# Performance work log

Hardware: AMD Instinct MI355X
Metric: run time of the kernel (lower is better)

The kernel has to match this reference:

```python
import jax, jax.numpy as jnp
import numpy as np

HEADS = 4
DIM_HEAD = 32
GROUPS = 32  # min(256//4, 32)
EPS = 1e-5


def setup_inputs() -> dict:
    key = jax.random.key(0)
    ks = jax.random.split(key, 5)
    B, C, H, W = 16, 256, 64, 64
    CD, HC, WC = 512, 32, 32
    hid = HEADS * DIM_HEAD  # 128
    return {
        "x": jax.random.normal(ks[0], (B, C, H, W), jnp.float32),
        "cond": jax.random.normal(ks[1], (B, CD, HC, WC), jnp.float32),
        "gn_w": jnp.ones((C,), jnp.float32),
        "gn_b": jnp.zeros((C,), jnp.float32),
        "w_q": jax.random.normal(ks[2], (hid, C), jnp.float32) * 0.05,
        "b_q": jnp.zeros((hid,), jnp.float32),
        "w_kv": jax.random.normal(ks[3], (2 * hid, CD), jnp.float32) * 0.05,
        "b_kv": jnp.zeros((2 * hid,), jnp.float32),
        "w_out": jax.random.normal(ks[4], (C, hid), jnp.float32) * 0.05,
        "b_out": jnp.zeros((C,), jnp.float32),
    }


def _group_norm(x, w, b):
    # x: (B, C, H, W); normalize per group over (channels-in-group, H, W)
    B, C, H, W = x.shape
    xg = x.reshape(B, GROUPS, C // GROUPS, H, W)
    mu = jnp.mean(xg, axis=(2, 3, 4), keepdims=True)
    var = jnp.var(xg, axis=(2, 3, 4), keepdims=True)
    xn = ((xg - mu) * jax.lax.rsqrt(var + EPS)).reshape(B, C, H, W)
    return xn * w[None, :, None, None] + b[None, :, None, None]


def _conv1x1(x, w, b):
    # x: (B, Cin, H, W), w: (Cout, Cin), b: (Cout,)
    return jnp.einsum('oc,bchw->bohw', w, x) + b[None, :, None, None]


def reference(x, cond, gn_w, gn_b, w_q, b_q, w_kv, b_kv, w_out, b_out):
    B, C, H, W = x.shape
    hid = HEADS * DIM_HEAD
    xn = _group_norm(x, gn_w, gn_b)
    q = _conv1x1(xn, w_q, b_q)          # (B, hid, H, W)
    kv = _conv1x1(cond, w_kv, b_kv)     # (B, 2*hid, Hc, Wc)
    Nc = kv.shape[2] * kv.shape[3]
    N = H * W
    k = kv[:, :hid].reshape(B, HEADS, DIM_HEAD, Nc)
    v = kv[:, hid:].reshape(B, HEADS, DIM_HEAD, Nc)
    q = q.reshape(B, HEADS, DIM_HEAD, N)
    k = jax.nn.softmax(k, axis=-1)
    # kv outer product: (B, heads, d, e)
    context = jnp.einsum('bhdn,bhen->bhde', k, v)
    # query contraction over d: (B, heads, e, n)
    out = jnp.einsum('bhde,bhdn->bhen', context, q)
    out = out.reshape(B, hid, H, W)
    return _conv1x1(out, w_out, b_out)
```

## Files before the change

### kernel.cpp

```cpp
#include <hip/hip_runtime.h>
#include <hip/hip_bf16.h>

typedef __attribute__((ext_vector_type(8))) short bf16x8;
typedef __attribute__((ext_vector_type(4))) float f32x4;

__device__ __forceinline__ ushort f2bf(float f) {
    __hip_bfloat16 h = __float2bfloat16(f);
    return __builtin_bit_cast(ushort, h);
}
__device__ __forceinline__ unsigned pack2(float a, float b) {
    return (unsigned)f2bf(a) | ((unsigned)f2bf(b) << 16);
}
__device__ __forceinline__ float bflo(unsigned u) { return __uint_as_float(u << 16); }
__device__ __forceinline__ float bfhi(unsigned u) { return __uint_as_float(u & 0xffff0000u); }

__device__ __forceinline__ void unpack8(uint4 r, float* o) {
    o[0] = bflo(r.x); o[1] = bfhi(r.x); o[2] = bflo(r.y); o[3] = bfhi(r.y);
    o[4] = bflo(r.z); o[5] = bfhi(r.z); o[6] = bflo(r.w); o[7] = bfhi(r.w);
}

__global__ __launch_bounds__(256) void kv_gemm(const float* __restrict__ w_kv,
                                               const float* __restrict__ cond,
                                               const float* __restrict__ b_kv,
                                               ushort* __restrict__ kv16,
                                               float* __restrict__ zbase) {
    __shared__ ushort lA[128 * 64];
    __shared__ ushort lB[32 * 64];
    __shared__ float scratch[64 * 32];
    int nc = blockIdx.x, rb = blockIdx.y, b = blockIdx.z;
    int t = threadIdx.x;
    int fid = blockIdx.x + 32 * (blockIdx.y + 2 * blockIdx.z);
    if (fid < 264) zbase[fid * 256 + t] = 0.f;
    int col0 = nc * 32, row0 = rb * 128;
    int l = t & 63, w = t >> 6;
    int lr = l & 15, lg = l >> 4;
    const float* Ab32 = w_kv + (size_t)row0 * 512;
    const float* Bb = cond + (size_t)b * 512 * 1024 + col0;
    int rA = t >> 3, gAr = t & 7, gw = gAr ^ (rA & 7);
    int rB = t >> 3, gB = t & 7;
    int sp = t & 31, sj4 = (t >> 5) & 7;
    float4 ka0_, ka1_, ka2_, ka3_, ka4_, ka5_, ka6_, ka7_;
    float4 kb0_, kb1_;
#define KG_LOADA(k0) { \
    ka0_ = *(const float4*)&Ab32[(size_t)(rA)      * 512 + (k0) + gAr * 8]; \
    ka1_ = *(const float4*)&Ab32[(size_t)(rA)      * 512 + (k0) + gAr * 8 + 4]; \
    ka2_ = *(const float4*)&Ab32[(size_t)(32 + rA) * 512 + (k0) + gAr * 8]; \
    ka3_ = *(const float4*)&Ab32[(size_t)(32 + rA) * 512 + (k0) + gAr * 8 + 4]; \
    ka4_ = *(const float4*)&Ab32[(size_t)(64 + rA) * 512 + (k0) + gAr * 8]; \
    ka5_ = *(const float4*)&Ab32[(size_t)(64 + rA) * 512 + (k0) + gAr * 8 + 4]; \
    ka6_ = *(const float4*)&Ab32[(size_t)(96 + rA) * 512 + (k0) + gAr * 8]; \
    ka7_ = *(const float4*)&Ab32[(size_t)(96 + rA) * 512 + (k0) + gAr * 8 + 4]; }
#define KG_LOADB(k0) { \
    kb0_ = *(const float4*)&Bb[(size_t)((k0) + rB)      * 1024 + gB * 4]; \
    kb1_ = *(const float4*)&Bb[(size_t)((k0) + 32 + rB) * 1024 + gB * 4]; }
#define KG_WRITEA() { uint4 p; \
    p.x = pack2(ka0_.x, ka0_.y); p.y = pack2(ka0_.z, ka0_.w); \
    p.z = pack2(ka1_.x, ka1_.y); p.w = pack2(ka1_.z, ka1_.w); \
    *(uint4*)((char*)lA + (size_t)((rA)      * 8 + gw) * 16) = p; \
    p.x = pack2(ka2_.x, ka2_.y); p.y = pack2(ka2_.z, ka2_.w); \
    p.z = pack2(ka3_.x, ka3_.y); p.w = pack2(ka3_.z, ka3_.w); \
    *(uint4*)((char*)lA + (size_t)((32 + rA) * 8 + gw) * 16) = p; \
    p.x = pack2(ka4_.x, ka4_.y); p.y = pack2(ka4_.z, ka4_.w); \
    p.z = pack2(ka5_.x, ka5_.y); p.w = pack2(ka5_.z, ka5_.w); \
    *(uint4*)((char*)lA + (size_t)((64 + rA) * 8 + gw) * 16) = p; \
    p.x = pack2(ka6_.x, ka6_.y); p.y = pack2(ka6_.z, ka6_.w); \
    p.z = pack2(ka7_.x, ka7_.y); p.w = pack2(ka7_.z, ka7_.w); \
    *(uint4*)((char*)lA + (size_t)((96 + rA) * 8 + gw) * 16) = p; }
#define KG_WRITEB() { \
    *(float4*)((char*)scratch + (rB)      * 128 + ((gB ^ (((rB)      >> 1) & 7)) * 16)) = kb0_; \
    *(float4*)((char*)scratch + (32 + rB) * 128 + ((gB ^ (((32 + rB) >> 1) & 7)) * 16)) = kb1_; }
#define KG_PACKB() { \
    int js = sj4 ^ (sp & 7); \
    float4 s0 = *(const float4*)((char*)scratch + (2*sp)   * 128 + js * 16); \
    float4 s2 = *(const float4*)((char*)scratch + (2*sp+1) * 128 + js * 16); \
    float c0v[4] = {s0.x, s0.y, s0.z, s0.w}; \
    float c1v[4] = {s2.x, s2.y, s2.z, s2.w}; \
    _Pragma("unroll") \
    for (int w4 = 0; w4 < 4; ++w4) { \
        int n = sj4 * 4 + w4; \
        unsigned pk = pack2(c0v[w4], c1v[w4]); \
        *(unsigned*)((char*)lB + n * 128 + (((sp >> 2) ^ (n & 7)) * 16) + (sp & 3) * 4) = pk; \
    } }
    KG_LOADA(0); KG_LOADB(0);
    f32x4 acc[2][2] = {};
    for (int it = 0; it < 8; ++it) {
        KG_WRITEA();
        KG_WRITEB();
        __syncthreads();
        if (it < 7) { KG_LOADA(it * 64 + 64); KG_LOADB(it * 64 + 64); }
        KG_PACKB();
        __syncthreads();
        #pragma unroll
        for (int ks = 0; ks < 2; ++ks) {
            bf16x8 av[2], bv[2];
            #pragma unroll
            for (int mi = 0; mi < 2; ++mi) {
                int ar = w * 32 + mi * 16 + lr;
                int q = (ks * 4 + lg) ^ (ar & 7);
                av[mi] = *(const bf16x8*)((const char*)lA + ar * 128 + q * 16);
            }
            #pragma unroll
            for (int ni = 0; ni < 2; ++ni) {
                int br = ni * 16 + lr;
                int q = (ks * 4 + lg) ^ (br & 7);
                bv[ni] = *(const bf16x8*)((const char*)lB + br * 128 + q * 16);
            }
            #pragma unroll
            for (int mi = 0; mi < 2; ++mi)
                #pragma unroll
                for (int ni = 0; ni < 2; ++ni)
                    acc[mi][ni] = __builtin_amdgcn_mfma_f32_16x16x32_bf16(
                        av[mi], bv[ni], acc[mi][ni], 0, 0, 0);
        }
        __syncthreads();
    }
#undef KG_LOADA
#undef KG_LOADB
#undef KG_WRITEA
#undef KG_WRITEB
#undef KG_PACKB
    int orow = row0 + w * 32;
    #pragma unroll
    for (int mi = 0; mi < 2; ++mi) {
        int rbase = orow + mi * 16 + lg * 4;
        float4 b4 = *(const float4*)&b_kv[rbase];
        float bvr[4] = {b4.x, b4.y, b4.z, b4.w};
        #pragma unroll
        for (int ni = 0; ni < 2; ++ni) {
            int cc = col0 + ni * 16 + lr;
            #pragma unroll
            for (int r = 0; r < 4; ++r)
                kv16[((size_t)b * 256 + rbase + r) * 1024 + cc] = f2bf(acc[mi][ni][r] + bvr[r]);
        }
    }
}

__global__ __launch_bounds__(256) void ctxstats_kernel(const ushort* __restrict__ kv,
                                                       const float* __restrict__ x,
                                                       float* __restrict__ rowsum,
                                                       float* __restrict__ ctx,
                                                       float* __restrict__ statacc) {
    __shared__ float pl[32][129], vl[32][129];
    int bid = blockIdx.x, t = threadIdx.x;
    if (bid < 512) {
        int bh = bid >> 3, b = bh >> 2, h = bh & 3;
        int n0 = (bid & 7) * 128;
        int r = t >> 3, cs = (t & 7) * 16;
        const ushort* kp = kv + ((size_t)b * 256 + h * 32 + r) * 1024 + n0 + cs;
        const ushort* vp = kv + ((size_t)b * 256 + 128 + h * 32 + r) * 1024 + n0 + cs;
        float kvals[16], vvals[16];
        unpack8(((const uint4*)kp)[0], kvals);
        unpack8(((const uint4*)kp)[1], kvals + 8);
        unpack8(((const uint4*)vp)[0], vvals);
        unpack8(((const uint4*)vp)[1], vvals + 8);
        float psum = 0.f;
        #pragma unroll
        for (int i = 0; i < 16; ++i) {
            float e = __expf(kvals[i]);
            pl[r][cs + i] = e;
            vl[r][cs + i] = vvals[i];
            psum += e;
        }
        psum += __shfl_xor(psum, 1, 64);
        psum += __shfl_xor(psum, 2, 64);
        psum += __shfl_xor(psum, 4, 64);
        if ((t & 7) == 0) atomicAdd(&rowsum[bh * 32 + r], psum);
        __syncthreads();
        int d0 = t >> 5, e0 = t & 31;
        float acc[4] = {0.f, 0.f, 0.f, 0.f};
        #pragma unroll 8
        for (int nn = 0; nn < 128; ++nn) {
            float vv = vl[e0][nn];
            #pragma unroll
            for (int i = 0; i < 4; ++i)
                acc[i] += pl[d0 + 8 * i][nn] * vv;
        }
        #pragma unroll
        for (int i = 0; i < 4; ++i)
            atomicAdd(&ctx[((size_t)bh * 32 + d0 + 8 * i) * 32 + e0], acc[i]);
    } else {
        int bg = bid - 512;
        const float4* xp = (const float4*)(x + (size_t)bg * 32768);
        float s = 0.f, ss = 0.f;
        #pragma unroll
        for (int j = 0; j < 32; ++j) {
            float4 v = xp[t + 256 * j];
            s  += v.x + v.y + v.z + v.w;
            ss += v.x*v.x + v.y*v.y + v.z*v.z + v.w*v.w;
        }
        #pragma unroll
        for (int off = 32; off > 0; off >>= 1) {
            s  += __shfl_down(s, off, 64);
            ss += __shfl_down(ss, off, 64);
        }
        int wave = t >> 6;
        if ((t & 63) == 0) { pl[0][wave * 2] = s; pl[0][wave * 2 + 1] = ss; }
        __syncthreads();
        if (t == 0) {
            statacc[bg * 2]     = pl[0][0] + pl[0][2] + pl[0][4] + pl[0][6];
            statacc[bg * 2 + 1] = pl[0][1] + pl[0][3] + pl[0][5] + pl[0][7];
        }
    }
}

__global__ __launch_bounds__(256) void a_kernel(const float* __restrict__ ctx,
                                                const float* __restrict__ rowsum,
                                                const float* __restrict__ w_out,
                                                const float* __restrict__ w_q,
                                                const float* __restrict__ b_q,
                                                const float* __restrict__ b_out,
                                                ushort* __restrict__ A16,
                                                float* __restrict__ biasb) {
    __shared__ float ctxl[4][32][33];
    __shared__ float wol[16][128];
    __shared__ float ml[16][128];
    int b = blockIdx.x >> 4, ot = (blockIdx.x & 15) << 4;
    int t = threadIdx.x;
    #pragma unroll
    for (int j = 0; j < 16; ++j) {
        int e = t + 256 * j;
        float inv = 1.f / rowsum[b * 128 + (e >> 5)];
        ctxl[e >> 10][(e >> 5) & 31][e & 31] = ctx[(size_t)b * 4096 + e] * inv;
    }
    #pragma unroll
    for (int j = 0; j < 8; ++j) {
        int e = t + 256 * j;
        wol[e >> 7][e & 127] = w_out[(ot + (e >> 7)) * 128 + (e & 127)];
    }
    __syncthreads();
    #pragma unroll
    for (int j = 0; j < 8; ++j) {
        int e = t + 256 * j;
        int o = e >> 7, hd = e & 127, h = hd >> 5, d = hd & 31;
        float acc = 0.f;
        #pragma unroll
        for (int ee = 0; ee < 32; ++ee) acc += wol[o][h * 32 + ee] * ctxl[h][d][ee];
        ml[o][hd] = acc;
    }
    __syncthreads();
    int c = t;
    float wt[16];
    #pragma unroll
    for (int o = 0; o < 16; ++o) wt[o] = 0.f;
    for (int hd = 0; hd < 128; ++hd) {
        float wq = w_q[hd * 256 + c];
        #pragma unroll
        for (int o = 0; o < 16; ++o) wt[o] += ml[o][hd] * wq;
    }
    ushort* Abp = A16 + ((size_t)b * 256 + ot) * 256 + c;
    #pragma unroll
    for (int o = 0; o < 16; ++o)
        Abp[(size_t)o * 256] = f2bf(wt[o]);
    if (t < 16) {
        int o = t;
        float md = 0.f;
        #pragma unroll 8
        for (int hd = 0; hd < 128; ++hd) md += ml[o][hd] * b_q[hd];
        biasb[(size_t)b * 256 + ot + o] = md + b_out[ot + o];
    }
}

__global__ __launch_bounds__(512) void out_gemm_fused(const ushort* __restrict__ A16,
                                                      const float* __restrict__ x,
                                                      const float* __restrict__ statacc,
                                                      const float* __restrict__ gn_w,
                                                      const float* __restrict__ gn_b,
                                                      const float* __restrict__ biasb,
                                                      float* __restrict__ out) {
    __shared__ ushort lA[256 * 64];
    __shared__ ushort lB[128 * 64];
    __shared__ float scratch[64 * 128];
    __shared__ float sct[256][2];
    int b = blockIdx.y;
    int n0 = blockIdx.x * 128;
    int t = threadIdx.x;
    int l = t & 63, wid = t >> 6;
    int wr = wid >> 1, wc = wid & 1;
    int lr = l & 15, lg = l >> 4;
    const ushort* Ab = A16 + (size_t)b * 65536;
    const float* xb = x + (size_t)b * 256 * 4096 + n0;
    int sp = t & 31, sj = t >> 5;
    if (t < 256) {
        int g = t >> 3;
        float S  = statacc[(b * 32 + g) * 2];
        float SS = statacc[(b * 32 + g) * 2 + 1];
        float mu  = S * (1.f / 32768.f);
        float var = SS * (1.f / 32768.f) - mu * mu;
        float sc = rsqrtf(var + 1e-5f) * gn_w[t];
        sct[t][0] = sc;
        sct[t][1] = gn_b[t] - mu * sc;
    }
    uint4 a0_, a1_, a2_, a3_;
    float4 b0_, b1_, b2_, b3_;
    int rA = t >> 3, gA = (t & 7) ^ (rA & 7);
    int rB = t >> 5, gB = t & 31;
#define OG_LOADA(k0) { \
    a0_ = *(const uint4*)(Ab + (size_t)(rA)       * 256 + (k0) + gA * 8); \
    a1_ = *(const uint4*)(Ab + (size_t)(64 + rA)  * 256 + (k0) + gA * 8); \
    a2_ = *(const uint4*)(Ab + (size_t)(128 + rA) * 256 + (k0) + gA * 8); \
    a3_ = *(const uint4*)(Ab + (size_t)(192 + rA) * 256 + (k0) + gA * 8); }
#define OG_LOADB(k0) { \
    b0_ = *(const float4*)&xb[(size_t)((k0) + rB)      * 4096 + gB * 4]; \
    b1_ = *(const float4*)&xb[(size_t)((k0) + 16 + rB) * 4096 + gB * 4]; \
    b2_ = *(const float4*)&xb[(size_t)((k0) + 32 + rB) * 4096 + gB * 4]; \
    b3_ = *(const float4*)&xb[(size_t)((k0) + 48 + rB) * 4096 + gB * 4]; }
    OG_LOADA(0); OG_LOADB(0);
    f32x4 acc[4][4] = {};
    for (int it = 0; it < 4; ++it) {
        int k0 = it * 64;
        *(uint4*)((char*)lA + (size_t)t * 16)          = a0_;
        *(uint4*)((char*)lA + (size_t)(512 + t) * 16)  = a1_;
        *(uint4*)((char*)lA + (size_t)(1024 + t) * 16) = a2_;
        *(uint4*)((char*)lA + (size_t)(1536 + t) * 16) = a3_;
        *(float4*)((char*)scratch + (rB)      * 512 + (gB ^ (((rB)      >> 1) & 31)) * 16) = b0_;
        *(float4*)((char*)scratch + (16 + rB) * 512 + (gB ^ (((16 + rB) >> 1) & 31)) * 16) = b1_;
        *(float4*)((char*)scratch + (32 + rB) * 512 + (gB ^ (((32 + rB) >> 1) & 31)) * 16) = b2_;
        *(float4*)((char*)scratch + (48 + rB) * 512 + (gB ^ (((48 + rB) >> 1) & 31)) * 16) = b3_;
        __syncthreads();
        if (it < 3) { OG_LOADA(k0 + 64); OG_LOADB(k0 + 64); }
        {
            int swz = sp & 31;
            float sc0 = sct[k0 + 2 * sp][0],     tc0 = sct[k0 + 2 * sp][1];
            float sc1 = sct[k0 + 2 * sp + 1][0], tc1 = sct[k0 + 2 * sp + 1][1];
            float4 s0 = *(const float4*)((char*)scratch + (2*sp)   * 512 + ((2*sj)   ^ swz) * 16);
            float4 s1 = *(const float4*)((char*)scratch + (2*sp)   * 512 + ((2*sj+1) ^ swz) * 16);
            float4 s2 = *(const float4*)((char*)scratch + (2*sp+1) * 512 + ((2*sj)   ^ swz) * 16);
            float4 s3 = *(const float4*)((char*)scratch + (2*sp+1) * 512 + ((2*sj+1) ^ swz) * 16);
            float c0v[8] = {s0.x, s0.y, s0.z, s0.w, s1.x, s1.y, s1.z, s1.w};
            float c1v[8] = {s2.x, s2.y, s2.z, s2.w, s3.x, s3.y, s3.z, s3.w};
            #pragma unroll
            for (int w = 0; w < 8; ++w) {
                int n = sj * 8 + w;
                unsigned pk = pack2(c0v[w] * sc0 + tc0, c1v[w] * sc1 + tc1);
                *(unsigned*)((char*)lB + n * 128 + (((sp >> 2) ^ (n & 7)) * 16) + (sp & 3) * 4) = pk;
            }
        }
        __syncthreads();
        #pragma unroll
        for (int ks = 0; ks < 2; ++ks) {
            bf16x8 av[4], bv[4];
            #pragma unroll
            for (int mi = 0; mi < 4; ++mi) {
                int ar = wr * 64 + mi * 16 + lr;
                int q = (ks * 4 + lg) ^ (ar & 7);
                av[mi] = *(const bf16x8*)((const char*)lA + ar * 128 + q * 16);
            }
            #pragma unroll
            for (int ni = 0; ni < 4; ++ni) {
                int br = wc * 64 + ni * 16 + lr;
                int q = (ks * 4 + lg) ^ (br & 7);
                bv[ni] = *(const bf16x8*)((const char*)lB + br * 128 + q * 16);
            }
            #pragma unroll
            for (int mi = 0; mi < 4; ++mi)
                #pragma unroll
                for (int ni = 0; ni < 4; ++ni)
                    acc[mi][ni] = __builtin_amdgcn_mfma_f32_16x16x32_bf16(
                        av[mi], bv[ni], acc[mi][ni], 0, 0, 0);
        }
        __syncthreads();
    }
#undef OG_LOADA
#undef OG_LOADB
    const float* bp = biasb + (size_t)b * 256;
    int orow = wr * 64, ocol = n0 + wc * 64 + lr;
    #pragma unroll
    for (int mi = 0; mi < 4; ++mi) {
        int rb = orow + mi * 16 + lg * 4;
        float4 b4 = *(const float4*)&bp[rb];
        float bvr[4] = {b4.x, b4.y, b4.z, b4.w};
        #pragma unroll
        for (int ni = 0; ni < 4; ++ni) {
            int cc = ocol + ni * 16;
            #pragma unroll
            for (int r = 0; r < 4; ++r)
                out[((size_t)b * 256 + rb + r) * 4096 + cc] = acc[mi][ni][r] + bvr[r];
        }
    }
}

extern "C" void kernel_launch(void* const* d_in, const int* in_sizes, int n_in,
                              void* d_out, int out_size, void* d_ws, size_t ws_size,
                              hipStream_t stream) {
    const float* x     = (const float*)d_in[0];
    const float* cond  = (const float*)d_in[1];
    const float* gn_w  = (const float*)d_in[2];
    const float* gn_b  = (const float*)d_in[3];
    const float* w_q   = (const float*)d_in[4];
    const float* b_q   = (const float*)d_in[5];
    const float* w_kv  = (const float*)d_in[6];
    const float* b_kv  = (const float*)d_in[7];
    const float* w_out = (const float*)d_in[8];
    const float* b_out = (const float*)d_in[9];
    float* out = (float*)d_out;

    float* f       = (float*)d_ws;
    float* statacc = f;
    float* rowsum  = f + 1024;
    float* ctx     = f + 3072;
    float* biasb   = f + 68608;
    ushort* u      = (ushort*)(f + 72704);
    ushort* kv16   = u;
    ushort* A16    = u + 4194304;

    kv_gemm<<<dim3(32, 2, 16), 256, 0, stream>>>(w_kv, cond, b_kv, kv16, rowsum);
    ctxstats_kernel<<<1024, 256, 0, stream>>>(kv16, x, rowsum, ctx, statacc);
    a_kernel<<<256, 256, 0, stream>>>(ctx, rowsum, w_out, w_q, b_q, b_out, A16, biasb);
    out_gemm_fused<<<dim3(32, 16), 512, 0, stream>>>(A16, x, statacc, gn_w, gn_b, biasb, out);
}
```

Measured before the change: 81.29 us.

## Halve out_gemm N-tile to 64 columns and raise wave priority around MFMA loops

The fused output GEMM now covers 64 spatial columns per block instead of 128. The grid doubles to 1024 blocks, and the LDS staging, swizzle and transpose-pack of x are reworked for the narrower tile. This is meant to give more blocks per CU and better occupancy and latency hiding, at the cost of reloading the 256x256 A matrix twice as often. It also wraps the MFMA inner loops in both GEMMs with s_setprio(1)/s_setprio(0) so waves doing math are favoured over waves that are loading.

```diff
diff --git a/kernel.cpp b/kernel.cpp
--- a/kernel.cpp
+++ b/kernel.cpp
@@ -90,6 +90,7 @@
         if (it < 7) { KG_LOADA(it * 64 + 64); KG_LOADB(it * 64 + 64); }
         KG_PACKB();
         __syncthreads();
+        __builtin_amdgcn_s_setprio(1);
         #pragma unroll
         for (int ks = 0; ks < 2; ++ks) {
             bf16x8 av[2], bv[2];
@@ -112,6 +113,7 @@
                     acc[mi][ni] = __builtin_amdgcn_mfma_f32_16x16x32_bf16(
                         av[mi], bv[ni], acc[mi][ni], 0, 0, 0);
         }
+        __builtin_amdgcn_s_setprio(0);
         __syncthreads();
     }
 #undef KG_LOADA
@@ -268,18 +270,18 @@
                                                       const float* __restrict__ biasb,
                                                       float* __restrict__ out) {
     __shared__ ushort lA[256 * 64];
-    __shared__ ushort lB[128 * 64];
-    __shared__ float scratch[64 * 128];
+    __shared__ ushort lB[64 * 64];
+    __shared__ float scratch[64 * 64];
     __shared__ float sct[256][2];
     int b = blockIdx.y;
-    int n0 = blockIdx.x * 128;
+    int n0 = blockIdx.x * 64;
     int t = threadIdx.x;
     int l = t & 63, wid = t >> 6;
     int wr = wid >> 1, wc = wid & 1;
     int lr = l & 15, lg = l >> 4;
     const ushort* Ab = A16 + (size_t)b * 65536;
     const float* xb = x + (size_t)b * 256 * 4096 + n0;
-    int sp = t & 31, sj = t >> 5;
+    int sp = t & 31, sj4 = t >> 5;
     if (t < 256) {
         int g = t >> 3;
         float S  = statacc[(b * 32 + g) * 2];
@@ -291,9 +293,9 @@
         sct[t][1] = gn_b[t] - mu * sc;
     }
     uint4 a0_, a1_, a2_, a3_;
-    float4 b0_, b1_, b2_, b3_;
+    float4 b0_, b1_;
     int rA = t >> 3, gA = (t & 7) ^ (rA & 7);
-    int rB = t >> 5, gB = t & 31;
+    int rB = t >> 4, gB = t & 15;
 #define OG_LOADA(k0) { \
     a0_ = *(const uint4*)(Ab + (size_t)(rA)       * 256 + (k0) + gA * 8); \
     a1_ = *(const uint4*)(Ab + (size_t)(64 + rA)  * 256 + (k0) + gA * 8); \
@@ -301,44 +303,39 @@
     a3_ = *(const uint4*)(Ab + (size_t)(192 + rA) * 256 + (k0) + gA * 8); }
 #define OG_LOADB(k0) { \
     b0_ = *(const float4*)&xb[(size_t)((k0) + rB)      * 4096 + gB * 4]; \
-    b1_ = *(const float4*)&xb[(size_t)((k0) + 16 + rB) * 4096 + gB * 4]; \
-    b2_ = *(const float4*)&xb[(size_t)((k0) + 32 + rB) * 4096 + gB * 4]; \
-    b3_ = *(const float4*)&xb[(size_t)((k0) + 48 + rB) * 4096 + gB * 4]; }
+    b1_ = *(const float4*)&xb[(size_t)((k0) + 32 + rB) * 4096 + gB * 4]; }
     OG_LOADA(0); OG_LOADB(0);
-    f32x4 acc[4][4] = {};
+    f32x4 acc[4][2] = {};
     for (int it = 0; it < 4; ++it) {
         int k0 = it * 64;
         *(uint4*)((char*)lA + (size_t)t * 16)          = a0_;
         *(uint4*)((char*)lA + (size_t)(512 + t) * 16)  = a1_;
         *(uint4*)((char*)lA + (size_t)(1024 + t) * 16) = a2_;
         *(uint4*)((char*)lA + (size_t)(1536 + t) * 16) = a3_;
-        *(float4*)((char*)scratch + (rB)      * 512 + (gB ^ (((rB)      >> 1) & 31)) * 16) = b0_;
-        *(float4*)((char*)scratch + (16 + rB) * 512 + (gB ^ (((16 + rB) >> 1) & 31)) * 16) = b1_;
-        *(float4*)((char*)scratch + (32 + rB) * 512 + (gB ^ (((32 + rB) >> 1) & 31)) * 16) = b2_;
-        *(float4*)((char*)scratch + (48 + rB) * 512 + (gB ^ (((48 + rB) >> 1) & 31)) * 16) = b3_;
+        *(float4*)((char*)scratch + (rB)      * 256 + ((gB ^ (((rB)      >> 1) & 15)) * 16)) = b0_;
+        *(float4*)((char*)scratch + (32 + rB) * 256 + ((gB ^ (((32 + rB) >> 1) & 15)) * 16)) = b1_;
         __syncthreads();
         if (it < 3) { OG_LOADA(k0 + 64); OG_LOADB(k0 + 64); }
         {
-            int swz = sp & 31;
+            int js = sj4 ^ (sp & 15);
             float sc0 = sct[k0 + 2 * sp][0],     tc0 = sct[k0 + 2 * sp][1];
             float sc1 = sct[k0 + 2 * sp + 1][0], tc1 = sct[k0 + 2 * sp + 1][1];
-            float4 s0 = *(const float4*)((char*)scratch + (2*sp)   * 512 + ((2*sj)   ^ swz) * 16);
-            float4 s1 = *(const float4*)((char*)scratch + (2*sp)   * 512 + ((2*sj+1) ^ swz) * 16);
-            float4 s2 = *(const float4*)((char*)scratch + (2*sp+1) * 512 + ((2*sj)   ^ swz) * 16);
-            float4 s3 = *(const float4*)((char*)scratch + (2*sp+1) * 512 + ((2*sj+1) ^ swz) * 16);
-            float c0v[8] = {s0.x, s0.y, s0.z, s0.w, s1.x, s1.y, s1.z, s1.w};
-            float c1v[8] = {s2.x, s2.y, s2.z, s2.w, s3.x, s3.y, s3.z, s3.w};
-            #pragma unroll
-            for (int w = 0; w < 8; ++w) {
-                int n = sj * 8 + w;
-                unsigned pk = pack2(c0v[w] * sc0 + tc0, c1v[w] * sc1 + tc1);
+            float4 s0 = *(const float4*)((char*)scratch + (2*sp)   * 256 + js * 16);
+            float4 s2 = *(const float4*)((char*)scratch + (2*sp+1) * 256 + js * 16);
+            float c0v[4] = {s0.x, s0.y, s0.z, s0.w};
+            float c1v[4] = {s2.x, s2.y, s2.z, s2.w};
+            #pragma unroll
+            for (int w4 = 0; w4 < 4; ++w4) {
+                int n = sj4 * 4 + w4;
+                unsigned pk = pack2(c0v[w4] * sc0 + tc0, c1v[w4] * sc1 + tc1);
                 *(unsigned*)((char*)lB + n * 128 + (((sp >> 2) ^ (n & 7)) * 16) + (sp & 3) * 4) = pk;
             }
         }
         __syncthreads();
+        __builtin_amdgcn_s_setprio(1);
         #pragma unroll
         for (int ks = 0; ks < 2; ++ks) {
-            bf16x8 av[4], bv[4];
+            bf16x8 av[4], bv[2];
             #pragma unroll
             for (int mi = 0; mi < 4; ++mi) {
                 int ar = wr * 64 + mi * 16 + lr;
@@ -346,35 +343,36 @@
                 av[mi] = *(const bf16x8*)((const char*)lA + ar * 128 + q * 16);
             }
             #pragma unroll
-            for (int ni = 0; ni < 4; ++ni) {
-                int br = wc * 64 + ni * 16 + lr;
+            for (int ni = 0; ni < 2; ++ni) {
+                int br = wc * 32 + ni * 16 + lr;
                 int q = (ks * 4 + lg) ^ (br & 7);
                 bv[ni] = *(const bf16x8*)((const char*)lB + br * 128 + q * 16);
             }
             #pragma unroll
             for (int mi = 0; mi < 4; ++mi)
                 #pragma unroll
-                for (int ni = 0; ni < 4; ++ni)
+                for (int ni = 0; ni < 2; ++ni)
                     acc[mi][ni] = __builtin_amdgcn_mfma_f32_16x16x32_bf16(
                         av[mi], bv[ni], acc[mi][ni], 0, 0, 0);
         }
+        __builtin_amdgcn_s_setprio(0);
         __syncthreads();
     }
 #undef OG_LOADA
 #undef OG_LOADB
     const float* bp = biasb + (size_t)b * 256;
-    int orow = wr * 64, ocol = n0 + wc * 64 + lr;
+    int orow = wr * 64, ocol = n0 + wc * 32 + lr;
     #pragma unroll
     for (int mi = 0; mi < 4; ++mi) {
-        int rb = orow + mi * 16 + lg * 4;
-        float4 b4 = *(const float4*)&bp[rb];
+        int rb2 = orow + mi * 16 + lg * 4;
+        float4 b4 = *(const float4*)&bp[rb2];
         float bvr[4] = {b4.x, b4.y, b4.z, b4.w};
         #pragma unroll
-        for (int ni = 0; ni < 4; ++ni) {
+        for (int ni = 0; ni < 2; ++ni) {
             int cc = ocol + ni * 16;
             #pragma unroll
             for (int r = 0; r < 4; ++r)
-                out[((size_t)b * 256 + rb + r) * 4096 + cc] = acc[mi][ni][r] + bvr[r];
+                out[((size_t)b * 256 + rb2 + r) * 4096 + cc] = acc[mi][ni][r] + bvr[r];
         }
     }
 }
@@ -406,5 +404,5 @@
     kv_gemm<<<dim3(32, 2, 16), 256, 0, stream>>>(w_kv, cond, b_kv, kv16, rowsum);
     ctxstats_kernel<<<1024, 256, 0, stream>>>(kv16, x, rowsum, ctx, statacc);
     a_kernel<<<256, 256, 0, stream>>>(ctx, rowsum, w_out, w_q, b_q, b_out, A16, biasb);
-    out_gemm_fused<<<dim3(32, 16), 512, 0, stream>>>(A16, x, statacc, gn_w, gn_b, biasb, out);
-}
+    out_gemm_fused<<<dim3(64, 16), 512, 0, stream>>>(A16, x, statacc, gn_w, gn_b, biasb, out);
+}
```

After: 78.80 us. -3.1%, faster.
